# Kernel optimization log

Hardware: AMD Instinct MI355X
Metric: run time of the kernel (lower is better)

Reference implementation:

```python
import jax, jax.numpy as jnp
import numpy as np

N = 50000
IN_F = 128
OUT_F = 128
NRELA = 128
E1 = 400000
E2 = 100000
ALPHA = 0.2   # LeakyReLU slope
D = 0.85      # PageRank damping
EPS = 1e-12


def setup_inputs() -> dict:
    key = jax.random.key(0)
    ks = jax.random.split(key, 8)
    return {
        "input": jax.random.normal(ks[0], (N, IN_F), dtype=jnp.float32),
        "edge": jax.random.randint(ks[1], (2, E1), 0, N, dtype=jnp.int64),
        "edge_embed": jax.random.normal(ks[2], (E1, NRELA), dtype=jnp.float32),
        "edge_list_nhop": jax.random.randint(ks[3], (2, E2), 0, N, dtype=jnp.int64),
        "edge_embed_nhop": jax.random.normal(ks[4], (E2, NRELA), dtype=jnp.float32),
        "entity_rank": jax.random.uniform(ks[5], (N,), dtype=jnp.float32),
        "a": 0.05 * jax.random.normal(ks[6], (OUT_F, 2 * IN_F + NRELA), dtype=jnp.float32),
        "a_2": 0.05 * jax.random.normal(ks[7], (1, OUT_F), dtype=jnp.float32),
    }


def reference(input, edge, edge_embed, edge_list_nhop, edge_embed_nhop, entity_rank, a, a_2):
    n = input.shape[0]
    # concat n-hop edges (len(edge_list_nhop) != 0 path in the original)
    e = jnp.concatenate([edge, edge_list_nhop], axis=1)          # [2, E]
    emb = jnp.concatenate([edge_embed, edge_embed_nhop], axis=0) # [E, nrela]
    src, dst = e[0], e[1]

    # edge MLP: edge_h = [x_src | x_dst | rel]  -> a @ edge_h^T, leakyrelu
    edge_h = jnp.concatenate([input[src], input[dst], emb], axis=1)   # [E, 2*in+nrela]
    edge_m = jax.nn.leaky_relu(edge_h @ a.T, ALPHA)                   # [E, out]
    powers = -jax.nn.leaky_relu(edge_m @ a_2[0], ALPHA)               # [E]
    edge_e = jnp.exp(powers)                                          # [E]

    # softmax-like normalization over incoming edges of each target node
    a_rowsum = jax.ops.segment_sum(edge_e, dst, num_segments=n)       # [N]
    a_rowsum = jnp.where(a_rowsum == 0.0, EPS, a_rowsum)
    rel_att = edge_e / a_rowsum[dst]                                  # [E]

    # PageRank-style rank update
    e_rowsum = jax.ops.segment_sum(rel_att, src, num_segments=n)      # [N] (out-sum)
    e_rowsum = jnp.where(e_rowsum == 0.0, EPS, e_rowsum)
    val = rel_att * entity_rank[src] / e_rowsum[src]                  # [E]
    e_colsum = jax.ops.segment_sum(val, dst, num_segments=n)          # [N]
    new_rank = 1.0 - D + D * e_colsum                                 # [N]

    # rank-weighted attention propagation of edge features
    edge_prop = (rel_att * new_rank[src])[:, None] * edge_m           # [E, out]
    h_prime = jax.ops.segment_sum(edge_prop, dst, num_segments=n)     # [N, out]

    return jax.nn.elu(h_prime), new_rank
```

## Files before the change

### kernel.cpp

```cpp
#include <hip/hip_runtime.h>
#include <math.h>

#define N_NODES 50000
#define E1N 400000
#define E2N 100000
#define E_TOT 500000
#define ALPHAC 0.2f
#define DAMP 0.85f
#define EPSC 1e-12f

typedef __bf16 bf16_t;
typedef __bf16 bf16x4 __attribute__((ext_vector_type(4)));
typedef __bf16 bf16x8 __attribute__((ext_vector_type(8)));
typedef _Float16 f16_t;
typedef _Float16 f16x4 __attribute__((ext_vector_type(4)));
typedef _Float16 f16x8 __attribute__((ext_vector_type(8)));
typedef float f32x16 __attribute__((ext_vector_type(16)));

__device__ __forceinline__ float lrelu(float x) { return x > 0.f ? x : ALPHAC * x; }

__global__ __launch_bounds__(256) void k_pack12(const float* __restrict__ a,
                                                bf16_t* __restrict__ bp) {
  int i = blockIdx.x * 256 + threadIdx.x;
  if (i >= 32768) return;
  int j = i & 7;
  int l = (i >> 3) & 63;
  int nt = (i >> 9) & 7;
  int ks = i >> 12;
  int c = nt * 32 + (l & 31);
  int o = (c < 128) ? c : c - 128;
  int koff = (c < 128) ? 0 : 128;
  int k = ks * 16 + ((l >> 5) << 3) + j;
  bp[i] = (bf16_t)a[o * 384 + koff + k];
}

__global__ __launch_bounds__(256) void k_pack3(const float* __restrict__ a,
                                               bf16_t* __restrict__ bp) {
  int i = blockIdx.x * 256 + threadIdx.x;
  if (i >= 16384) return;
  int j = i & 7;
  int l = (i >> 3) & 63;
  int nt = (i >> 9) & 3;
  int ks = i >> 11;
  int o = nt * 32 + (l & 31);
  int k = ks * 16 + ((l >> 5) << 3) + j;
  bp[i] = (bf16_t)a[o * 384 + 256 + k];
}

__global__ __launch_bounds__(256) void k_edges(const int* __restrict__ edge,
                                               const int* __restrict__ nhop,
                                               int* __restrict__ sidx,
                                               int* __restrict__ didx, int stride,
                                               int* __restrict__ cnt) {
  int e = blockIdx.x * 256 + threadIdx.x;
  if (e >= E_TOT) return;
  int s, d;
  if (e < E1N) {
    s = edge[(size_t)e * stride];
    d = edge[(size_t)(E1N + e) * stride];
  } else {
    int t = e - E1N;
    s = nhop[(size_t)t * stride];
    d = nhop[(size_t)(E2N + t) * stride];
  }
  sidx[e] = s;
  didx[e] = d;
  if (cnt) atomicAdd(&cnt[d], 1);
}

__global__ __launch_bounds__(256) void k_scan(const int* __restrict__ cnt,
                                              int* __restrict__ csr_start,
                                              int* __restrict__ cursor) {
  __shared__ int ls[256];
  __shared__ int lofs[256];
  int t = threadIdx.x;
  int lo = t * 196, hi = lo + 196;
  if (hi > N_NODES) hi = N_NODES;
  int s = 0;
  for (int i = lo; i < hi; ++i) s += cnt[i];
  ls[t] = s;
  __syncthreads();
  if (t == 0) {
    int run = 0;
    for (int i = 0; i < 256; ++i) { lofs[i] = run; run += ls[i]; }
  }
  __syncthreads();
  int run = lofs[t];
  for (int i = lo; i < hi; ++i) {
    csr_start[i] = run;
    cursor[i] = run;
    run += cnt[i];
  }
}

__global__ __launch_bounds__(256) void k_pos(const int* __restrict__ didx,
                                             int* __restrict__ cursor,
                                             int* __restrict__ eid) {
  int e = blockIdx.x * 256 + threadIdx.x;
  if (e >= E_TOT) return;
  int pos = atomicAdd(&cursor[didx[e]], 1);
  eid[pos] = e;
}

__global__ __launch_bounds__(256) void k_uv(const float* __restrict__ input,
                                            const bf16_t* __restrict__ bp12,
                                            bf16_t* __restrict__ uv) {
  const int tid = threadIdx.x, lane = tid & 63, wv = tid >> 6;
  const int n0 = blockIdx.x * 128 + wv * 32;
  const int m = lane & 31, hi2 = lane >> 5;
  int n = n0 + m;
  if (n >= N_NODES) n = 0;
  const float* ar = input + (size_t)n * 128 + hi2 * 8;
  const bf16x8* bp = (const bf16x8*)bp12;

  f32x16 acc[8];
#pragma unroll
  for (int nt = 0; nt < 8; ++nt)
#pragma unroll
    for (int r = 0; r < 16; ++r) acc[nt][r] = 0.f;

#pragma unroll
  for (int ks = 0; ks < 8; ++ks) {
    float4 u0 = *(const float4*)(ar + ks * 16);
    float4 u1 = *(const float4*)(ar + ks * 16 + 4);
    bf16x8 af = {(bf16_t)u0.x, (bf16_t)u0.y, (bf16_t)u0.z, (bf16_t)u0.w,
                 (bf16_t)u1.x, (bf16_t)u1.y, (bf16_t)u1.z, (bf16_t)u1.w};
#pragma unroll
    for (int nt = 0; nt < 8; ++nt)
      acc[nt] = __builtin_amdgcn_mfma_f32_32x32x16_bf16(af, bp[(ks * 8 + nt) * 64 + lane],
                                                        acc[nt], 0, 0, 0);
  }
#pragma unroll
  for (int nt = 0; nt < 8; ++nt)
#pragma unroll
    for (int r = 0; r < 16; ++r) {
      int row = (r & 3) + ((r >> 2) << 3) + (hi2 << 2);
      int node = n0 + row;
      if (node < N_NODES) uv[(size_t)node * 256 + nt * 32 + m] = (bf16_t)acc[nt][r];
    }
}

__global__ __launch_bounds__(256, 4) void k_gemm3(const float* __restrict__ eemb,
                                                  const float* __restrict__ eembn,
                                                  const bf16_t* __restrict__ bp3,
                                                  f16_t* __restrict__ w3) {
  __shared__ __align__(16) char s_raw[32768];
  const int tid = threadIdx.x;
  const long long e0 = (long long)blockIdx.x * 128;

  {
    const int r8 = tid >> 5;
    const int cb = (tid & 31) * 8;
#pragma unroll
    for (int i = 0; i < 16; ++i) {
      int row = i * 8 + r8;
      long long e = e0 + row;
      float4 u = {0.f, 0.f, 0.f, 0.f};
      if (e < E_TOT) {
        const float* src = (e < E1N) ? eemb + (size_t)e * 128
                                     : eembn + (size_t)(e - E1N) * 128;
        u = *(const float4*)(src + (cb >> 1));
      }
      bf16x4 b = {(bf16_t)u.x, (bf16_t)u.y, (bf16_t)u.z, (bf16_t)u.w};
      *(bf16x4*)(s_raw + row * 256 + (cb ^ ((row & 7) << 4))) = b;
    }
  }
  __syncthreads();

  const int lane = tid & 63, wv = tid >> 6;
  const int m = lane & 31, hi2 = lane >> 5;
  const int arow = wv * 32 + m;
  const int swz = (arow & 7) << 4;
  const bf16x8* bp = (const bf16x8*)bp3;

  f32x16 acc[4];
#pragma unroll
  for (int nt = 0; nt < 4; ++nt)
#pragma unroll
    for (int r = 0; r < 16; ++r) acc[nt][r] = 0.f;

  bf16x8 bb[4], bn[4];
#pragma unroll
  for (int nt = 0; nt < 4; ++nt) bb[nt] = bp[nt * 64 + lane];

#pragma unroll
  for (int ks = 0; ks < 8; ++ks) {
    bf16x8 af = *(const bf16x8*)(s_raw + arow * 256 + ((ks * 32 + hi2 * 16) ^ swz));
    if (ks < 7) {
#pragma unroll
      for (int nt = 0; nt < 4; ++nt) bn[nt] = bp[((ks + 1) * 4 + nt) * 64 + lane];
    }
#pragma unroll
    for (int nt = 0; nt < 4; ++nt)
      acc[nt] = __builtin_amdgcn_mfma_f32_32x32x16_bf16(af, bb[nt], acc[nt], 0, 0, 0);
#pragma unroll
    for (int nt = 0; nt < 4; ++nt) bb[nt] = bn[nt];
  }
  __syncthreads();

#pragma unroll
  for (int nt = 0; nt < 4; ++nt)
#pragma unroll
    for (int r = 0; r < 16; ++r) {
      int orow = (r & 3) + ((r >> 2) << 3) + (hi2 << 2);
      int row = wv * 32 + orow;
      int cb = (nt * 32 + m) * 2;
      *(f16_t*)(s_raw + row * 256 + (cb ^ ((row & 7) << 4))) = (f16_t)acc[nt][r];
    }
  __syncthreads();

  {
    const int rr = tid >> 4;
    const int cb = (tid & 15) * 16;
#pragma unroll
    for (int i = 0; i < 8; ++i) {
      int row = i * 16 + rr;
      long long e = e0 + row;
      if (e < E_TOT) {
        f16x8 v = *(const f16x8*)(s_raw + row * 256 + (cb ^ ((row & 7) << 4)));
        *(f16x8*)(w3 + (size_t)e * 128 + (cb >> 1)) = v;
      }
    }
  }
}

__global__ __launch_bounds__(256) void k_passB(const bf16_t* __restrict__ uv,
                                               const int* __restrict__ sidx,
                                               const int* __restrict__ didx,
                                               f16_t* __restrict__ w3,
                                               const float* __restrict__ a2,
                                               float* __restrict__ edge_e,
                                               float* __restrict__ a_rowsum) {
  long long e = (long long)blockIdx.x * 8 + (threadIdx.x >> 5);
  if (e >= E_TOT) return;
  const int m = threadIdx.x & 31;
  int s = sidx[e], d = didx[e];
  bf16x4 u = *(const bf16x4*)(uv + (size_t)s * 256 + m * 4);
  bf16x4 v = *(const bf16x4*)(uv + (size_t)d * 256 + 128 + m * 4);
  f16x4 w = *(const f16x4*)(w3 + (size_t)e * 128 + m * 4);
  float4 a2v = *(const float4*)(a2 + m * 4);
  float p0 = lrelu((float)u[0] + (float)v[0] + (float)w[0]);
  float p1 = lrelu((float)u[1] + (float)v[1] + (float)w[1]);
  float p2 = lrelu((float)u[2] + (float)v[2] + (float)w[2]);
  float p3 = lrelu((float)u[3] + (float)v[3] + (float)w[3]);
  bf16x4 po = {(bf16_t)p0, (bf16_t)p1, (bf16_t)p2, (bf16_t)p3};
  *(f16x4*)(w3 + (size_t)e * 128 + m * 4) = __builtin_bit_cast(f16x4, po);
  float sac = p0 * a2v.x + p1 * a2v.y + p2 * a2v.z + p3 * a2v.w;
#pragma unroll
  for (int off = 1; off < 32; off <<= 1) sac += __shfl_xor(sac, off, 64);
  if (m == 0) {
    float ev = expf(-lrelu(sac));
    edge_e[e] = ev;
    atomicAdd(&a_rowsum[d], ev);
  }
}

__global__ __launch_bounds__(256) void k_hprime(const bf16_t* __restrict__ P,
                                                const int* __restrict__ eid,
                                                const int* __restrict__ csr_start,
                                                const int* __restrict__ cnt,
                                                const float* __restrict__ rel_att,
                                                const int* __restrict__ sidx,
                                                const float* __restrict__ new_rank,
                                                float* __restrict__ out) {
  int g = (blockIdx.x << 3) | (threadIdx.x >> 5);
  if (g >= N_NODES) return;
  int m = threadIdx.x & 31;
  int start = csr_start[g], deg = cnt[g];
  float a0 = 0.f, a1 = 0.f, a2v = 0.f, a3v = 0.f;
  for (int i = 0; i < deg; ++i) {
    int e = eid[start + i];
    float we = rel_att[e] * new_rank[sidx[e]];
    bf16x4 p = *(const bf16x4*)(P + (size_t)e * 128 + m * 4);
    a0 += we * (float)p[0];
    a1 += we * (float)p[1];
    a2v += we * (float)p[2];
    a3v += we * (float)p[3];
  }
  float4 r;
  r.x = a0 > 0.f ? a0 : expm1f(a0);
  r.y = a1 > 0.f ? a1 : expm1f(a1);
  r.z = a2v > 0.f ? a2v : expm1f(a2v);
  r.w = a3v > 0.f ? a3v : expm1f(a3v);
  *(float4*)(out + (size_t)g * 128 + m * 4) = r;
}

template <bool ACCUM>
__global__ __launch_bounds__(256, 3) void k_pass(
    const float* __restrict__ eemb, const float* __restrict__ eembn,
    const bf16_t* __restrict__ uv, const int* __restrict__ sidx,
    const int* __restrict__ didx, const bf16_t* __restrict__ bp3,
    const float* __restrict__ a2, float* __restrict__ edge_e,
    float* __restrict__ a_rowsum, const float* __restrict__ rel_att,
    const float* __restrict__ new_rank, float* __restrict__ hout) {
  __shared__ bf16_t s_sum[128][136];
  const int tid = threadIdx.x;
  const long long e0 = (long long)blockIdx.x * 128;
  {
    const int g = tid >> 5;
    const int cl = (tid & 31) * 4;
#pragma unroll
    for (int i = 0; i < 16; ++i) {
      int el = i * 8 + g;
      long long e = e0 + el;
      float sx = 0.f, sy = 0.f, sz = 0.f, sw = 0.f;
      if (e < E_TOT) {
        int s = sidx[e], d = didx[e];
        bf16x4 u = *(const bf16x4*)(uv + (size_t)s * 256 + cl);
        bf16x4 v = *(const bf16x4*)(uv + (size_t)d * 256 + 128 + cl);
        sx = (float)u[0] + (float)v[0];
        sy = (float)u[1] + (float)v[1];
        sz = (float)u[2] + (float)v[2];
        sw = (float)u[3] + (float)v[3];
      }
      bf16x4 o = {(bf16_t)sx, (bf16_t)sy, (bf16_t)sz, (bf16_t)sw};
      *(bf16x4*)&s_sum[el][cl] = o;
    }
  }
  __syncthreads();

  const int lane = tid & 63;
  const int wv = tid >> 6;
  const long long e0w = e0 + wv * 32;
  if (e0w >= E_TOT) return;
  const int m = lane & 31, hi2 = lane >> 5;
  const long long e = e0w + m;
  const float* b2 = (e < E1N) ? (eemb + (size_t)e * 128)
                              : (eembn + (size_t)(e - E1N) * 128);
  const float* ar = b2 + hi2 * 8;

  const bf16x8* bp = (const bf16x8*)bp3;
  f32x16 acc[4];
#pragma unroll
  for (int nt = 0; nt < 4; ++nt)
#pragma unroll
    for (int r = 0; r < 16; ++r) acc[nt][r] = 0.f;

  auto loadA = [&](int ks) -> bf16x8 {
    float4 u0 = *(const float4*)(ar + ks * 16);
    float4 u1 = *(const float4*)(ar + ks * 16 + 4);
    bf16x8 rr = {(bf16_t)u0.x, (bf16_t)u0.y, (bf16_t)u0.z, (bf16_t)u0.w,
                 (bf16_t)u1.x, (bf16_t)u1.y, (bf16_t)u1.z, (bf16_t)u1.w};
    return rr;
  };

  bf16x8 a_cur = loadA(0);
  bf16x8 bb[4], bn[4];
#pragma unroll
  for (int nt = 0; nt < 4; ++nt) bb[nt] = bp[nt * 64 + lane];

#pragma unroll
  for (int ks = 0; ks < 8; ++ks) {
    bf16x8 a_nxt;
    if (ks < 7) {
      a_nxt = loadA(ks + 1);
#pragma unroll
      for (int nt = 0; nt < 4; ++nt) bn[nt] = bp[((ks + 1) * 4 + nt) * 64 + lane];
    }
#pragma unroll
    for (int nt = 0; nt < 4; ++nt)
      acc[nt] = __builtin_amdgcn_mfma_f32_32x32x16_bf16(a_cur, bb[nt], acc[nt], 0, 0, 0);
    a_cur = a_nxt;
#pragma unroll
    for (int nt = 0; nt < 4; ++nt) bb[nt] = bn[nt];
  }

  if (!ACCUM) {
    float sac[16];
#pragma unroll
    for (int r = 0; r < 16; ++r) sac[r] = 0.f;
#pragma unroll
    for (int nt = 0; nt < 4; ++nt) {
      float a2v = a2[nt * 32 + m];
      int o = nt * 32 + m;
#pragma unroll
      for (int r = 0; r < 16; ++r) {
        int row = (r & 3) + ((r >> 2) << 3) + (hi2 << 2);
        float c = acc[nt][r] + (float)s_sum[wv * 32 + row][o];
        sac[r] += lrelu(c) * a2v;
      }
    }
#pragma unroll
    for (int off = 1; off < 32; off <<= 1) {
#pragma unroll
      for (int r = 0; r < 16; ++r) sac[r] += __shfl_xor(sac[r], off, 64);
    }
    if (m == 0) {
#pragma unroll
      for (int r = 0; r < 16; ++r) {
        int row = (r & 3) + ((r >> 2) << 3) + (hi2 << 2);
        long long ee_i = e0w + row;
        float ev = expf(-lrelu(sac[r]));
        edge_e[ee_i] = ev;
        atomicAdd(&a_rowsum[didx[ee_i]], ev);
      }
    }
  } else {
    float w_m = rel_att[e] * new_rank[sidx[e]];
    int d = didx[e];
    float wr[16];
    int dr[16];
#pragma unroll
    for (int r = 0; r < 16; ++r) {
      int row = (r & 3) + ((r >> 2) << 3) + (hi2 << 2);
      wr[r] = __shfl(w_m, row, 64);
      dr[r] = __shfl(d, row, 64);
    }
#pragma unroll
    for (int nt = 0; nt < 4; ++nt) {
      int o = nt * 32 + m;
#pragma unroll
      for (int r = 0; r < 16; ++r) {
        int row = (r & 3) + ((r >> 2) << 3) + (hi2 << 2);
        float c = acc[nt][r] + (float)s_sum[wv * 32 + row][o];
        atomicAdd(&hout[(size_t)dr[r] * 128 + o], lrelu(c) * wr[r]);
      }
    }
  }
}

__global__ __launch_bounds__(256) void k_relatt(const float* __restrict__ edge_e,
                                                const int* __restrict__ didx,
                                                const int* __restrict__ sidx,
                                                const float* __restrict__ a_rowsum,
                                                float* __restrict__ rel_att,
                                                float* __restrict__ e_rowsum) {
  int e = blockIdx.x * 256 + threadIdx.x;
  if (e >= E_TOT) return;
  float rs = a_rowsum[didx[e]];
  rs = (rs == 0.f) ? EPSC : rs;
  float r = edge_e[e] / rs;
  rel_att[e] = r;
  atomicAdd(&e_rowsum[sidx[e]], r);
}

__global__ __launch_bounds__(256) void k_val(const float* __restrict__ rel_att,
                                             const int* __restrict__ sidx,
                                             const int* __restrict__ didx,
                                             const float* __restrict__ rank,
                                             const float* __restrict__ e_rowsum,
                                             float* __restrict__ e_colsum) {
  int e = blockIdx.x * 256 + threadIdx.x;
  if (e >= E_TOT) return;
  int s = sidx[e];
  float er = e_rowsum[s];
  er = (er == 0.f) ? EPSC : er;
  float val = rel_att[e] * rank[s] / er;
  atomicAdd(&e_colsum[didx[e]], val);
}

__global__ __launch_bounds__(256) void k_rank(const float* __restrict__ e_colsum,
                                              float* __restrict__ new_rank,
                                              float* __restrict__ out_tail) {
  int n = blockIdx.x * 256 + threadIdx.x;
  if (n >= N_NODES) return;
  float nr = 1.f - DAMP + DAMP * e_colsum[n];
  new_rank[n] = nr;
  out_tail[n] = nr;
}

__global__ __launch_bounds__(256) void k_elu(float* __restrict__ h) {
  int i = blockIdx.x * 256 + threadIdx.x;
  if (i < N_NODES * 128) {
    float x = h[i];
    h[i] = x > 0.f ? x : expm1f(x);
  }
}

extern "C" void kernel_launch(void* const* d_in, const int* in_sizes, int n_in,
                              void* d_out, int out_size, void* d_ws, size_t ws_size,
                              hipStream_t stream) {
  const float* input = (const float*)d_in[0];
  const int* edge = (const int*)d_in[1];
  const float* eemb = (const float*)d_in[2];
  const int* enh = (const int*)d_in[3];
  const float* eembn = (const float*)d_in[4];
  const float* rank = (const float*)d_in[5];
  const float* a = (const float*)d_in[6];
  const float* a2 = (const float*)d_in[7];
  float* out = (float*)d_out;

  int estride = (in_sizes[1] == 2 * E1N) ? 1 : 2;

  char* ws = (char*)d_ws;
  bf16_t* bp12 = (bf16_t*)(ws);
  bf16_t* bp3 = (bf16_t*)(ws + 65536);
  bf16_t* uv = (bf16_t*)(ws + 98304);
  int* sidx = (int*)(ws + 25698304);
  int* didx = (int*)(ws + 27698304);
  float* edge_e = (float*)(ws + 29698304);
  float* rel_att = (float*)(ws + 31698304);
  int* eid = (int*)(ws + 35698304);
  int* csr_start = (int*)(ws + 37698304);
  int* cursor = (int*)(ws + 37898304);
  int* cnt = (int*)(ws + 38098304);
  float* a_rowsum = (float*)(ws + 38298304);
  float* e_rowsum = (float*)(ws + 38498304);
  float* e_colsum = (float*)(ws + 38698304);
  float* new_rank = (float*)(ws + 38898304);
  bf16_t* P = (bf16_t*)(ws + 39098304);

  const bool big = ws_size >= 167098304ULL;

  const int NB = (E_TOT + 127) / 128;
  const int EB = (E_TOT + 255) / 256;

  if (big) {
    hipMemsetAsync(cnt, 0, 4 * 200000, stream);

    k_pack12<<<128, 256, 0, stream>>>(a, bp12);
    k_pack3<<<64, 256, 0, stream>>>(a, bp3);
    k_edges<<<EB, 256, 0, stream>>>(edge, enh, sidx, didx, estride, cnt);
    k_scan<<<1, 256, 0, stream>>>(cnt, csr_start, cursor);
    k_pos<<<EB, 256, 0, stream>>>(didx, cursor, eid);
    k_uv<<<(N_NODES + 127) / 128, 256, 0, stream>>>(input, bp12, uv);

    k_gemm3<<<NB, 256, 0, stream>>>(eemb, eembn, bp3, (f16_t*)P);
    k_passB<<<(E_TOT + 7) / 8, 256, 0, stream>>>(uv, sidx, didx, (f16_t*)P, a2,
                                                 edge_e, a_rowsum);
    k_relatt<<<EB, 256, 0, stream>>>(edge_e, didx, sidx, a_rowsum, rel_att, e_rowsum);
    k_val<<<EB, 256, 0, stream>>>(rel_att, sidx, didx, rank, e_rowsum, e_colsum);
    k_rank<<<(N_NODES + 255) / 256, 256, 0, stream>>>(e_colsum, new_rank,
                                                      out + (size_t)N_NODES * 128);
    k_hprime<<<(N_NODES + 7) / 8, 256, 0, stream>>>(P, eid, csr_start, cnt, rel_att,
                                                    sidx, new_rank, out);
  } else {
    hipMemsetAsync(cnt, 0, 4 * 200000, stream);
    hipMemsetAsync(out, 0, (size_t)N_NODES * 128 * 4, stream);

    k_pack12<<<128, 256, 0, stream>>>(a, bp12);
    k_pack3<<<64, 256, 0, stream>>>(a, bp3);
    k_edges<<<EB, 256, 0, stream>>>(edge, enh, sidx, didx, estride, nullptr);
    k_uv<<<(N_NODES + 127) / 128, 256, 0, stream>>>(input, bp12, uv);

    k_pass<false><<<NB, 256, 0, stream>>>(eemb, eembn, uv, sidx, didx, bp3, a2,
                                          edge_e, a_rowsum, nullptr, nullptr, nullptr);
    k_relatt<<<EB, 256, 0, stream>>>(edge_e, didx, sidx, a_rowsum, rel_att, e_rowsum);
    k_val<<<EB, 256, 0, stream>>>(rel_att, sidx, didx, rank, e_rowsum, e_colsum);
    k_rank<<<(N_NODES + 255) / 256, 256, 0, stream>>>(e_colsum, new_rank,
                                                      out + (size_t)N_NODES * 128);
    k_pass<true><<<NB, 256, 0, stream>>>(eemb, eembn, uv, sidx, didx, bp3, a2,
                                         nullptr, nullptr, rel_att, new_rank, out);
    k_elu<<<(N_NODES * 128 + 255) / 256, 256, 0, stream>>>(out);
  }
}
```

Before: 776.0 us.

## Fuse edge-embedding GEMM with per-edge attention pass into one kernel

Merges k_gemm3 and k_passB into a single kernel. The relation-embedding GEMM result stays in shared memory, and the gather/LeakyReLU/a_2 dot/exp/atomic work runs in the epilogue. This avoids writing the fp16 intermediate to global memory and reading it back, which is about 128 MB of round-trip traffic, and it drops one launch. The embedding loads are also batched into register arrays so that more loads are in flight. The cost is that the epilogue gathers (uv rows, indices, atomics) now run inside the occupancy-limited GEMM kernel.

```diff
diff --git a/kernel.cpp b/kernel.cpp
--- a/kernel.cpp
+++ b/kernel.cpp
@@ -14,7 +14,6 @@
 typedef __bf16 bf16x8 __attribute__((ext_vector_type(8)));
 typedef _Float16 f16_t;
 typedef _Float16 f16x4 __attribute__((ext_vector_type(4)));
-typedef _Float16 f16x8 __attribute__((ext_vector_type(8)));
 typedef float f32x16 __attribute__((ext_vector_type(16)));
 
 __device__ __forceinline__ float lrelu(float x) { return x > 0.f ? x : ALPHAC * x; }
@@ -140,10 +139,12 @@
     }
 }
 
-__global__ __launch_bounds__(256, 4) void k_gemm3(const float* __restrict__ eemb,
-                                                  const float* __restrict__ eembn,
-                                                  const bf16_t* __restrict__ bp3,
-                                                  f16_t* __restrict__ w3) {
+__global__ __launch_bounds__(256, 4) void k_passA2(
+    const float* __restrict__ eemb, const float* __restrict__ eembn,
+    const bf16_t* __restrict__ uv, const int* __restrict__ sidx,
+    const int* __restrict__ didx, const bf16_t* __restrict__ bp3,
+    const float* __restrict__ a2, float* __restrict__ edge_e,
+    float* __restrict__ a_rowsum, bf16_t* __restrict__ P) {
   __shared__ __align__(16) char s_raw[32768];
   const int tid = threadIdx.x;
   const long long e0 = (long long)blockIdx.x * 128;
@@ -152,17 +153,25 @@
     const int r8 = tid >> 5;
     const int cb = (tid & 31) * 8;
 #pragma unroll
-    for (int i = 0; i < 16; ++i) {
-      int row = i * 8 + r8;
-      long long e = e0 + row;
-      float4 u = {0.f, 0.f, 0.f, 0.f};
-      if (e < E_TOT) {
-        const float* src = (e < E1N) ? eemb + (size_t)e * 128
-                                     : eembn + (size_t)(e - E1N) * 128;
-        u = *(const float4*)(src + (cb >> 1));
-      }
-      bf16x4 b = {(bf16_t)u.x, (bf16_t)u.y, (bf16_t)u.z, (bf16_t)u.w};
-      *(bf16x4*)(s_raw + row * 256 + (cb ^ ((row & 7) << 4))) = b;
+    for (int c = 0; c < 2; ++c) {
+      float4 rg[8];
+#pragma unroll
+      for (int i = 0; i < 8; ++i) {
+        int row = (c * 8 + i) * 8 + r8;
+        long long e = e0 + row;
+        rg[i] = make_float4(0.f, 0.f, 0.f, 0.f);
+        if (e < E_TOT) {
+          const float* src = (e < E1N) ? eemb + (size_t)e * 128
+                                       : eembn + (size_t)(e - E1N) * 128;
+          rg[i] = *(const float4*)(src + (cb >> 1));
+        }
+      }
+#pragma unroll
+      for (int i = 0; i < 8; ++i) {
+        int row = (c * 8 + i) * 8 + r8;
+        bf16x4 b = {(bf16_t)rg[i].x, (bf16_t)rg[i].y, (bf16_t)rg[i].z, (bf16_t)rg[i].w};
+        *(bf16x4*)(s_raw + row * 256 + (cb ^ ((row & 7) << 4))) = b;
+      }
     }
   }
   __syncthreads();
@@ -210,48 +219,34 @@
   __syncthreads();
 
   {
-    const int rr = tid >> 4;
-    const int cb = (tid & 15) * 16;
-#pragma unroll
-    for (int i = 0; i < 8; ++i) {
-      int row = i * 16 + rr;
+    const int g = tid >> 5;
+    const int ml = tid & 31;
+    const int cl = ml * 4;
+    const float4 a2v = *(const float4*)(a2 + cl);
+#pragma unroll
+    for (int i = 0; i < 16; ++i) {
+      int row = i * 8 + g;
       long long e = e0 + row;
-      if (e < E_TOT) {
-        f16x8 v = *(const f16x8*)(s_raw + row * 256 + (cb ^ ((row & 7) << 4)));
-        *(f16x8*)(w3 + (size_t)e * 128 + (cb >> 1)) = v;
-      }
-    }
-  }
-}
-
-__global__ __launch_bounds__(256) void k_passB(const bf16_t* __restrict__ uv,
-                                               const int* __restrict__ sidx,
-                                               const int* __restrict__ didx,
-                                               f16_t* __restrict__ w3,
-                                               const float* __restrict__ a2,
-                                               float* __restrict__ edge_e,
-                                               float* __restrict__ a_rowsum) {
-  long long e = (long long)blockIdx.x * 8 + (threadIdx.x >> 5);
-  if (e >= E_TOT) return;
-  const int m = threadIdx.x & 31;
-  int s = sidx[e], d = didx[e];
-  bf16x4 u = *(const bf16x4*)(uv + (size_t)s * 256 + m * 4);
-  bf16x4 v = *(const bf16x4*)(uv + (size_t)d * 256 + 128 + m * 4);
-  f16x4 w = *(const f16x4*)(w3 + (size_t)e * 128 + m * 4);
-  float4 a2v = *(const float4*)(a2 + m * 4);
-  float p0 = lrelu((float)u[0] + (float)v[0] + (float)w[0]);
-  float p1 = lrelu((float)u[1] + (float)v[1] + (float)w[1]);
-  float p2 = lrelu((float)u[2] + (float)v[2] + (float)w[2]);
-  float p3 = lrelu((float)u[3] + (float)v[3] + (float)w[3]);
-  bf16x4 po = {(bf16_t)p0, (bf16_t)p1, (bf16_t)p2, (bf16_t)p3};
-  *(f16x4*)(w3 + (size_t)e * 128 + m * 4) = __builtin_bit_cast(f16x4, po);
-  float sac = p0 * a2v.x + p1 * a2v.y + p2 * a2v.z + p3 * a2v.w;
-#pragma unroll
-  for (int off = 1; off < 32; off <<= 1) sac += __shfl_xor(sac, off, 64);
-  if (m == 0) {
-    float ev = expf(-lrelu(sac));
-    edge_e[e] = ev;
-    atomicAdd(&a_rowsum[d], ev);
+      if (e >= E_TOT) break;
+      int s = sidx[e], d = didx[e];
+      bf16x4 uu = *(const bf16x4*)(uv + (size_t)s * 256 + cl);
+      bf16x4 vv = *(const bf16x4*)(uv + (size_t)d * 256 + 128 + cl);
+      f16x4 cc = *(const f16x4*)(s_raw + row * 256 + ((cl * 2) ^ ((row & 7) << 4)));
+      float p0 = lrelu((float)cc[0] + (float)uu[0] + (float)vv[0]);
+      float p1 = lrelu((float)cc[1] + (float)uu[1] + (float)vv[1]);
+      float p2 = lrelu((float)cc[2] + (float)uu[2] + (float)vv[2]);
+      float p3 = lrelu((float)cc[3] + (float)uu[3] + (float)vv[3]);
+      bf16x4 po = {(bf16_t)p0, (bf16_t)p1, (bf16_t)p2, (bf16_t)p3};
+      *(bf16x4*)(P + (size_t)e * 128 + cl) = po;
+      float sac = p0 * a2v.x + p1 * a2v.y + p2 * a2v.z + p3 * a2v.w;
+#pragma unroll
+      for (int off = 1; off < 32; off <<= 1) sac += __shfl_xor(sac, off, 64);
+      if (ml == 0) {
+        float ev = expf(-lrelu(sac));
+        edge_e[e] = ev;
+        atomicAdd(&a_rowsum[d], ev);
+      }
+    }
   }
 }
 
@@ -515,9 +510,8 @@
     k_pos<<<EB, 256, 0, stream>>>(didx, cursor, eid);
     k_uv<<<(N_NODES + 127) / 128, 256, 0, stream>>>(input, bp12, uv);
 
-    k_gemm3<<<NB, 256, 0, stream>>>(eemb, eembn, bp3, (f16_t*)P);
-    k_passB<<<(E_TOT + 7) / 8, 256, 0, stream>>>(uv, sidx, didx, (f16_t*)P, a2,
-                                                 edge_e, a_rowsum);
+    k_passA2<<<NB, 256, 0, stream>>>(eemb, eembn, uv, sidx, didx, bp3, a2,
+                                     edge_e, a_rowsum, P);
     k_relatt<<<EB, 256, 0, stream>>>(edge_e, didx, sidx, a_rowsum, rel_att, e_rowsum);
     k_val<<<EB, 256, 0, stream>>>(rel_att, sidx, didx, rank, e_rowsum, e_colsum);
     k_rank<<<(N_NODES + 255) / 256, 256, 0, stream>>>(e_colsum, new_rank,
```

Measured after the change: 787.3 us. No clear change (+1.5%).
